# Performance work log

Hardware: AMD Instinct MI355X
Metric: run time of the kernel (lower is better)

The kernel has to match this reference:

```python
import jax, jax.numpy as jnp
import numpy as np

N_NODES = 100000
N_EDGES = 600000
IN_DIM, HID, OUT = 6, 128, 1
EPS = 1e-5


def _glorot(key, shape):
    fan_in, fan_out = shape[1], shape[0]
    lim = jnp.sqrt(6.0 / (fan_in + fan_out))
    return jax.random.uniform(key, shape, jnp.float32, -lim, lim)


def setup_inputs() -> dict:
    key = jax.random.key(0)
    ks = jax.random.split(key, 16)
    x = jax.random.normal(ks[0], (N_NODES, IN_DIM), jnp.float32)
    edge_index = jax.random.randint(ks[1], (2, N_EDGES), 0, N_NODES, jnp.int64)
    return {
        "x": x,
        "edge_index": edge_index,
        # SAGEConv layer 0: 6 -> 128 (lin_l acts on aggregated neighbors, lin_r on root)
        "w_l0": _glorot(ks[2], (HID, IN_DIM)), "b_l0": jnp.zeros((HID,), jnp.float32),
        "w_r0": _glorot(ks[3], (HID, IN_DIM)),
        "bn_g0": jnp.ones((HID,), jnp.float32), "bn_b0": jnp.zeros((HID,), jnp.float32),
        # SAGEConv layer 1: 128 -> 128
        "w_l1": _glorot(ks[4], (HID, HID)), "b_l1": jnp.zeros((HID,), jnp.float32),
        "w_r1": _glorot(ks[5], (HID, HID)),
        "bn_g1": jnp.ones((HID,), jnp.float32), "bn_b1": jnp.zeros((HID,), jnp.float32),
        # SAGEConv layer 2: 128 -> 1
        "w_l2": _glorot(ks[6], (OUT, HID)), "b_l2": jnp.zeros((OUT,), jnp.float32),
        "w_r2": _glorot(ks[7], (OUT, HID)),
    }


def _sage_conv(x, src, dst, inv_deg, w_l, b_l, w_r):
    # mean aggregation of source-node features into destination nodes
    agg = jax.ops.segment_sum(x[src], dst, num_segments=N_NODES)  # [N, d]
    mean_nb = agg * inv_deg[:, None]
    return mean_nb @ w_l.T + b_l + x @ w_r.T


def _batch_norm(x, gamma, beta):
    mu = jnp.mean(x, axis=0)
    var = jnp.mean(jnp.square(x - mu), axis=0)  # biased, as torch BN training
    return (x - mu) * jax.lax.rsqrt(var + EPS) * gamma + beta


def reference(x, edge_index, w_l0, b_l0, w_r0, bn_g0, bn_b0,
              w_l1, b_l1, w_r1, bn_g1, bn_b1, w_l2, b_l2, w_r2):
    src, dst = edge_index[0], edge_index[1]
    deg = jax.ops.segment_sum(jnp.ones_like(dst, dtype=x.dtype), dst,
                              num_segments=N_NODES)
    inv_deg = 1.0 / jnp.maximum(deg, 1.0)

    h = _sage_conv(x, src, dst, inv_deg, w_l0, b_l0, w_r0)
    h = jax.nn.relu(_batch_norm(h, bn_g0, bn_b0))  # dropout = identity (eval)

    h = _sage_conv(h, src, dst, inv_deg, w_l1, b_l1, w_r1)
    h = jax.nn.relu(_batch_norm(h, bn_g1, bn_b1))

    h = _sage_conv(h, src, dst, inv_deg, w_l2, b_l2, w_r2)
    return jax.nn.sigmoid(h).squeeze(-1)  # [N]
```

## Files before the change

### kernel.cpp

```cpp
#include <hip/hip_runtime.h>
#include <math.h>

#define HID 128
#define INDIM 6

typedef float4 f4;
typedef __attribute__((ext_vector_type(8))) short short8;
typedef __attribute__((ext_vector_type(4))) float f32x4;

static __device__ inline unsigned short f2bf(float f) {
    union { float f; unsigned int u; } v; v.f = f;
    unsigned int r = v.u + 0x7fffu + ((v.u >> 16) & 1u);
    return (unsigned short)(r >> 16);
}
static __device__ inline float bf2f_lo(unsigned int u) {
    union { unsigned int u; float f; } v; v.u = u << 16; return v.f;
}
static __device__ inline float bf2f_hi(unsigned int u) {
    union { unsigned int u; float f; } v; v.u = u & 0xffff0000u; return v.f;
}

__global__ void k_init(int* a, int na, int* b, int nb,
                       const float* __restrict__ wl, const float* __restrict__ wr,
                       unsigned short* __restrict__ wcat) {
    int i = blockIdx.x * blockDim.x + threadIdx.x;
    if (i < na) a[i] = 0;
    if (i < nb) b[i] = 0;
    if (i < 32768) {
        int o = i >> 8, k = i & 255;
        float v = (k < 128) ? wl[o * 128 + k] : wr[o * 128 + k - 128];
        wcat[i] = f2bf(v);
    }
}

__global__ void k_deg(const int* dst, int* deg, int* rank, int E) {
    int e = blockIdx.x * blockDim.x + threadIdx.x;
    if (e < E) rank[e] = atomicAdd(&deg[dst[e]], 1);
}

__global__ void k_scan_partial(const int* __restrict__ deg, int* __restrict__ partial, int N) {
    __shared__ int lds[256];
    int t = threadIdx.x;
    int base = blockIdx.x * 1024 + t * 4;
    int s = 0;
    if (base + 4 <= N) {
        int4 v = *(const int4*)&deg[base];
        s = v.x + v.y + v.z + v.w;
    } else {
        for (int i = 0; i < 4; i++) if (base + i < N) s += deg[base + i];
    }
    lds[t] = s;
    __syncthreads();
    for (int off = 128; off > 0; off >>= 1) {
        if (t < off) lds[t] += lds[t + off];
        __syncthreads();
    }
    if (t == 0) partial[blockIdx.x] = lds[0];
}

__global__ void k_scan_write(const int* __restrict__ deg, const int* __restrict__ partial,
                             int* __restrict__ rowptr, float* __restrict__ invd,
                             int N, int E, int nb) {
    __shared__ int lds[256];
    __shared__ int ptot[256];
    int t = threadIdx.x;
    ptot[t] = (t < nb) ? partial[t] : 0;
    __syncthreads();
    for (int off = 1; off < 256; off <<= 1) {
        int v = (t >= off) ? ptot[t - off] : 0;
        __syncthreads();
        ptot[t] += v;
        __syncthreads();
    }
    int blockbase = (blockIdx.x == 0) ? 0 : ptot[blockIdx.x - 1];

    int base = blockIdx.x * 1024 + t * 4;
    int v0 = 0, v1 = 0, v2 = 0, v3 = 0;
    if (base + 4 <= N) {
        int4 v = *(const int4*)&deg[base];
        v0 = v.x; v1 = v.y; v2 = v.z; v3 = v.w;
    } else {
        if (base + 0 < N) v0 = deg[base + 0];
        if (base + 1 < N) v1 = deg[base + 1];
        if (base + 2 < N) v2 = deg[base + 2];
        if (base + 3 < N) v3 = deg[base + 3];
    }
    lds[t] = v0 + v1 + v2 + v3;
    __syncthreads();
    for (int off = 1; off < 256; off <<= 1) {
        int v = (t >= off) ? lds[t - off] : 0;
        __syncthreads();
        lds[t] += v;
        __syncthreads();
    }
    int run = blockbase + ((t == 0) ? 0 : lds[t - 1]);
    if (base + 0 < N) { rowptr[base + 0] = run; invd[base + 0] = 1.0f / (float)max(v0, 1); } run += v0;
    if (base + 1 < N) { rowptr[base + 1] = run; invd[base + 1] = 1.0f / (float)max(v1, 1); } run += v1;
    if (base + 2 < N) { rowptr[base + 2] = run; invd[base + 2] = 1.0f / (float)max(v2, 1); } run += v2;
    if (base + 3 < N) { rowptr[base + 3] = run; invd[base + 3] = 1.0f / (float)max(v3, 1); } run += v3;
    if (blockIdx.x == 0 && t == 0) rowptr[N] = E;
}

__global__ void k_fill(const int* ei, const int* rank, const int* rowptr, int* csr, int E) {
    int e = blockIdx.x * blockDim.x + threadIdx.x;
    if (e < E) {
        int d = ei[E + e];
        csr[rowptr[d] + rank[e]] = ei[e];
    }
}

__global__ __launch_bounds__(256) void k_l0stats(
        const float* __restrict__ x, const int* __restrict__ rowptr,
        const int* __restrict__ csr, const float* __restrict__ invd,
        const float* __restrict__ wl, const float* __restrict__ bl,
        const float* __restrict__ wr, float* __restrict__ mean6,
        float* __restrict__ sum8, float* __restrict__ sq8, int N) {
    __shared__ float wlds[1600];
    __shared__ float blds[136];
    __shared__ float mx[32][8];
    __shared__ float xr[32][8];
    __shared__ float ps[4][128];
    __shared__ float pq[4][128];
    int t = threadIdx.x;
    for (int idx = t; idx < 1536; idx += 256) {
        int half = idx >= 768 ? 1 : 0;
        int lin = idx - half * 768;
        int o = lin / 6, i = lin - o * 6;
        float v = half ? wr[lin] : wl[lin];
        wlds[half * 800 + o * 6 + i + (o >> 4) * 2] = v;
    }
    if (t < 128) blds[t + (t >> 4)] = bl[t];
    int nl = t >> 3, f = t & 7;
    int n = blockIdx.x * 32 + nl;
    bool valid = n < N;
    if (f < 6) {
        float mean = 0.f, xv = 0.f;
        if (valid) {
            int s = rowptr[n], e = rowptr[n + 1];
            float acc = 0.f;
            int i = s;
            for (; i + 4 <= e; i += 4) {
                int i0 = csr[i], i1 = csr[i + 1], i2 = csr[i + 2], i3 = csr[i + 3];
                float a0 = x[i0 * 6 + f], a1 = x[i1 * 6 + f];
                float a2 = x[i2 * 6 + f], a3 = x[i3 * 6 + f];
                acc += (a0 + a1) + (a2 + a3);
            }
            int rem = e - i;
            if (rem > 0) {
                int eL = e - 1;
                int i0 = csr[i];
                int i1 = csr[min(i + 1, eL)];
                int i2 = csr[min(i + 2, eL)];
                float a0 = x[i0 * 6 + f];
                float a1 = x[i1 * 6 + f];
                float a2 = x[i2 * 6 + f];
                acc += a0;
                if (rem > 1) acc += a1;
                if (rem > 2) acc += a2;
            }
            mean = acc * invd[n];
            xv = x[n * 6 + f];
            mean6[n * 6 + f] = mean;
        }
        mx[nl][f] = mean;
        xr[nl][f] = xv;
    }
    __syncthreads();
    float m0 = mx[nl][0], m1 = mx[nl][1], m2 = mx[nl][2];
    float m3 = mx[nl][3], m4 = mx[nl][4], m5 = mx[nl][5];
    float r0 = xr[nl][0], r1 = xr[nl][1], r2 = xr[nl][2];
    float r3 = xr[nl][3], r4 = xr[nl][4], r5 = xr[nl][5];
    const float* wA = wlds;
    const float* wB = wlds + 800;
    int wv = t >> 6, lane = t & 63;
#pragma unroll
    for (int k = 0; k < 16; k++) {
        int o = f * 16 + k;
        int wb = 98 * f + 6 * k;
        float h = blds[o + f];
        h += m0 * wA[wb] + m1 * wA[wb + 1] + m2 * wA[wb + 2]
           + m3 * wA[wb + 3] + m4 * wA[wb + 4] + m5 * wA[wb + 5];
        h += r0 * wB[wb] + r1 * wB[wb + 1] + r2 * wB[wb + 2]
           + r3 * wB[wb + 3] + r4 * wB[wb + 4] + r5 * wB[wb + 5];
        float s = valid ? h : 0.f;
        float q = s * s;
        s += __shfl_xor(s, 8, 64);  q += __shfl_xor(q, 8, 64);
        s += __shfl_xor(s, 16, 64); q += __shfl_xor(q, 16, 64);
        s += __shfl_xor(s, 32, 64); q += __shfl_xor(q, 32, 64);
        if (lane < 8) { ps[wv][lane * 16 + k] = s; pq[wv][lane * 16 + k] = q; }
    }
    __syncthreads();
    if (t < 128) {
        float S = ps[0][t] + ps[1][t] + ps[2][t] + ps[3][t];
        float Q = pq[0][t] + pq[1][t] + pq[2][t] + pq[3][t];
        int slot = (blockIdx.x & 7) * 128 + t;
        atomicAdd(&sum8[slot], S);
        atomicAdd(&sq8[slot], Q);
    }
}

__global__ __launch_bounds__(256) void k_l0apply(
        const float* __restrict__ x, const float* __restrict__ mean6,
        const float* __restrict__ wl, const float* __restrict__ bl,
        const float* __restrict__ wr, const float* __restrict__ sum8,
        const float* __restrict__ sq8, const float* __restrict__ g,
        const float* __restrict__ be, float invN,
        unsigned short* __restrict__ out, int N) {
    __shared__ float wlds[1600];
    __shared__ float blds[136];
    __shared__ float sclds[136];
    __shared__ float shlds[136];
    __shared__ float mx[32][8];
    __shared__ float xr[32][8];
    int t = threadIdx.x;
    for (int idx = t; idx < 1536; idx += 256) {
        int half = idx >= 768 ? 1 : 0;
        int lin = idx - half * 768;
        int o = lin / 6, i = lin - o * 6;
        float v = half ? wr[lin] : wl[lin];
        wlds[half * 800 + o * 6 + i + (o >> 4) * 2] = v;
    }
    if (t < 128) {
        blds[t + (t >> 4)] = bl[t];
        float s = 0.f, q = 0.f;
        for (int c = 0; c < 8; c++) { s += sum8[c * 128 + t]; q += sq8[c * 128 + t]; }
        float mu  = s * invN;
        float var = q * invN - mu * mu;
        float sc  = g[t] * rsqrtf(var + 1e-5f);
        sclds[t + (t >> 4)] = sc;
        shlds[t + (t >> 4)] = be[t] - mu * sc;
    }
    int nl = t >> 3, f = t & 7;
    int n = blockIdx.x * 32 + nl;
    bool valid = n < N;
    if (f < 6) {
        mx[nl][f] = valid ? mean6[n * 6 + f] : 0.f;
        xr[nl][f] = valid ? x[n * 6 + f] : 0.f;
    }
    __syncthreads();
    if (!valid) return;
    float m0 = mx[nl][0], m1 = mx[nl][1], m2 = mx[nl][2];
    float m3 = mx[nl][3], m4 = mx[nl][4], m5 = mx[nl][5];
    float r0 = xr[nl][0], r1 = xr[nl][1], r2 = xr[nl][2];
    float r3 = xr[nl][3], r4 = xr[nl][4], r5 = xr[nl][5];
    const float* wA = wlds;
    const float* wB = wlds + 800;
    unsigned short pk[16];
#pragma unroll
    for (int k4 = 0; k4 < 4; k4++) {
#pragma unroll
        for (int j = 0; j < 4; j++) {
            int k = k4 * 4 + j;
            int o = f * 16 + k;
            int wb = 98 * f + 6 * k;
            float h = blds[o + f];
            h += m0 * wA[wb] + m1 * wA[wb + 1] + m2 * wA[wb + 2]
               + m3 * wA[wb + 3] + m4 * wA[wb + 4] + m5 * wA[wb + 5];
            h += r0 * wB[wb] + r1 * wB[wb + 1] + r2 * wB[wb + 2]
               + r3 * wB[wb + 3] + r4 * wB[wb + 4] + r5 * wB[wb + 5];
            pk[k] = f2bf(fmaxf(0.f, fmaf(h, sclds[o + f], shlds[o + f])));
        }
    }
    unsigned short* dst = out + (size_t)n * HID + f * 16;
    *(uint4*)(dst)     = *(const uint4*)&pk[0];
    *(uint4*)(dst + 8) = *(const uint4*)&pk[8];
}

__global__ void k_agg_bf(const unsigned short* __restrict__ hb, const int* __restrict__ rowptr,
                         const int* __restrict__ csr, const float* __restrict__ invd,
                         unsigned short* __restrict__ out, int N) {
    int t = threadIdx.x;
    int w = t >> 6, lid = t & 63;
    int q = lid >> 4, l16 = lid & 15;
    int n = blockIdx.x * 16 + w * 4 + q;
    if (n >= N) return;
    int s = rowptr[n], e = rowptr[n + 1];
    const uint4* hb128 = (const uint4*)hb;
    float ax0 = 0.f, ay0 = 0.f, ax1 = 0.f, ay1 = 0.f;
    float ax2 = 0.f, ay2 = 0.f, ax3 = 0.f, ay3 = 0.f;
    int i = s;
    for (; i + 4 <= e; i += 4) {
        int i0 = csr[i], i1 = csr[i + 1], i2 = csr[i + 2], i3 = csr[i + 3];
        uint4 u0 = hb128[(size_t)i0 * 16 + l16];
        uint4 u1 = hb128[(size_t)i1 * 16 + l16];
        uint4 u2 = hb128[(size_t)i2 * 16 + l16];
        uint4 u3 = hb128[(size_t)i3 * 16 + l16];
        ax0 += (bf2f_lo(u0.x) + bf2f_lo(u1.x)) + (bf2f_lo(u2.x) + bf2f_lo(u3.x));
        ay0 += (bf2f_hi(u0.x) + bf2f_hi(u1.x)) + (bf2f_hi(u2.x) + bf2f_hi(u3.x));
        ax1 += (bf2f_lo(u0.y) + bf2f_lo(u1.y)) + (bf2f_lo(u2.y) + bf2f_lo(u3.y));
        ay1 += (bf2f_hi(u0.y) + bf2f_hi(u1.y)) + (bf2f_hi(u2.y) + bf2f_hi(u3.y));
        ax2 += (bf2f_lo(u0.z) + bf2f_lo(u1.z)) + (bf2f_lo(u2.z) + bf2f_lo(u3.z));
        ay2 += (bf2f_hi(u0.z) + bf2f_hi(u1.z)) + (bf2f_hi(u2.z) + bf2f_hi(u3.z));
        ax3 += (bf2f_lo(u0.w) + bf2f_lo(u1.w)) + (bf2f_lo(u2.w) + bf2f_lo(u3.w));
        ay3 += (bf2f_hi(u0.w) + bf2f_hi(u1.w)) + (bf2f_hi(u2.w) + bf2f_hi(u3.w));
    }
    int rem = e - i;
    if (rem > 0) {
        int eL = e - 1;
        int i0 = csr[i];
        int i1 = csr[min(i + 1, eL)];
        int i2 = csr[min(i + 2, eL)];
        uint4 u0 = hb128[(size_t)i0 * 16 + l16];
        uint4 u1 = hb128[(size_t)i1 * 16 + l16];
        uint4 u2 = hb128[(size_t)i2 * 16 + l16];
        ax0 += bf2f_lo(u0.x); ay0 += bf2f_hi(u0.x);
        ax1 += bf2f_lo(u0.y); ay1 += bf2f_hi(u0.y);
        ax2 += bf2f_lo(u0.z); ay2 += bf2f_hi(u0.z);
        ax3 += bf2f_lo(u0.w); ay3 += bf2f_hi(u0.w);
        if (rem > 1) {
            ax0 += bf2f_lo(u1.x); ay0 += bf2f_hi(u1.x);
            ax1 += bf2f_lo(u1.y); ay1 += bf2f_hi(u1.y);
            ax2 += bf2f_lo(u1.z); ay2 += bf2f_hi(u1.z);
            ax3 += bf2f_lo(u1.w); ay3 += bf2f_hi(u1.w);
        }
        if (rem > 2) {
            ax0 += bf2f_lo(u2.x); ay0 += bf2f_hi(u2.x);
            ax1 += bf2f_lo(u2.y); ay1 += bf2f_hi(u2.y);
            ax2 += bf2f_lo(u2.z); ay2 += bf2f_hi(u2.z);
            ax3 += bf2f_lo(u2.w); ay3 += bf2f_hi(u2.w);
        }
    }
    float id = invd[n];
    uint4 r;
    r.x = (unsigned int)f2bf(ax0 * id) | ((unsigned int)f2bf(ay0 * id) << 16);
    r.y = (unsigned int)f2bf(ax1 * id) | ((unsigned int)f2bf(ay1 * id) << 16);
    r.z = (unsigned int)f2bf(ax2 * id) | ((unsigned int)f2bf(ay2 * id) << 16);
    r.w = (unsigned int)f2bf(ax3 * id) | ((unsigned int)f2bf(ay3 * id) << 16);
    ((uint4*)out)[(size_t)n * 16 + l16] = r;
}

__global__ __launch_bounds__(256) void k_gemm(
        const unsigned short* __restrict__ Bm, const unsigned short* __restrict__ Ar,
        const unsigned short* __restrict__ wcat, const float* __restrict__ bias,
        float* __restrict__ sum8, float* __restrict__ sq8,
        unsigned short* __restrict__ C, int N) {
    __shared__ __align__(16) unsigned short As[64][72];
    __shared__ __align__(16) unsigned short Ws[128][72];
    __shared__ float lds_s[128];
    __shared__ float lds_q[128];
    int t = threadIdx.x;
    int wave = t >> 6, lane = t & 63;
    int row0 = blockIdx.x * 64;
    int lrow = lane & 15, koff = (lane >> 4) * 8;

    f32x4 acc[4][2];
#pragma unroll
    for (int m = 0; m < 4; m++)
#pragma unroll
        for (int n = 0; n < 2; n++) acc[m][n] = (f32x4)(0.f);

    for (int chunk = 0; chunk < 4; chunk++) {
        int kb = chunk * 64;
        int rA = t >> 2, qA = t & 3;
        int srow = row0 + rA;
        int cA = (kb & 127) + qA * 16;
        const unsigned short* src = (kb < 128) ? Bm : Ar;
        uint4 a0, a1;
        if (srow < N) {
            const unsigned short* p = src + (size_t)srow * HID + cA;
            a0 = *(const uint4*)(p); a1 = *(const uint4*)(p + 8);
        } else {
            a0 = a1 = make_uint4(0, 0, 0, 0);
        }
        *(uint4*)&As[rA][qA * 16]     = a0;
        *(uint4*)&As[rA][qA * 16 + 8] = a1;
        int rW = t >> 1, hW = t & 1;
        const unsigned short* wp = wcat + rW * 256 + kb + hW * 32;
        *(uint4*)&Ws[rW][hW * 32]      = *(const uint4*)(wp);
        *(uint4*)&Ws[rW][hW * 32 + 8]  = *(const uint4*)(wp + 8);
        *(uint4*)&Ws[rW][hW * 32 + 16] = *(const uint4*)(wp + 16);
        *(uint4*)&Ws[rW][hW * 32 + 24] = *(const uint4*)(wp + 24);
        __syncthreads();

#pragma unroll
        for (int ks = 0; ks < 64; ks += 32) {
            short8 af[4], bfr[2];
#pragma unroll
            for (int m = 0; m < 4; m++)
                af[m] = *(const short8*)&As[m * 16 + lrow][ks + koff];
#pragma unroll
            for (int n = 0; n < 2; n++)
                bfr[n] = *(const short8*)&Ws[wave * 32 + n * 16 + lrow][ks + koff];
#pragma unroll
            for (int m = 0; m < 4; m++)
#pragma unroll
                for (int n = 0; n < 2; n++)
                    acc[m][n] = __builtin_amdgcn_mfma_f32_16x16x32_bf16(af[m], bfr[n], acc[m][n], 0, 0, 0);
        }
        __syncthreads();
    }

    unsigned short* Cst = &Ws[0][0];
    int cl = lane & 15, rq = (lane >> 4) * 4;
#pragma unroll
    for (int n = 0; n < 2; n++) {
        int col = wave * 32 + n * 16 + cl;
        float bn = bias[col];
        float s = 0.f, q = 0.f;
#pragma unroll
        for (int m = 0; m < 4; m++) {
#pragma unroll
            for (int reg = 0; reg < 4; reg++) {
                int rl = m * 16 + rq + reg;
                float v = acc[m][n][reg] + bn;
                Cst[rl * 136 + col] = f2bf(v);
                if (row0 + rl < N) { s += v; q += v * v; }
            }
        }
        s += __shfl_xor(s, 16, 64); q += __shfl_xor(q, 16, 64);
        s += __shfl_xor(s, 32, 64); q += __shfl_xor(q, 32, 64);
        if (lane < 16) { lds_s[col] = s; lds_q[col] = q; }
    }
    __syncthreads();
    if (t < 128) {
        int slot = (blockIdx.x & 7) * 128 + t;
        atomicAdd(&sum8[slot], lds_s[t]);
        atomicAdd(&sq8[slot], lds_q[t]);
    }
#pragma unroll
    for (int j = 0; j < 4; j++) {
        int idx = t + j * 256;
        int rl = idx >> 4, seg = idx & 15;
        int row = row0 + rl;
        if (row < N)
            *(uint4*)(C + (size_t)row * HID + seg * 8) = *(const uint4*)&Cst[rl * 136 + seg * 8];
    }
}

__global__ void k_dots(const unsigned short* __restrict__ h, const float* __restrict__ sum8,
                       const float* __restrict__ sq8, const float* __restrict__ g,
                       const float* __restrict__ be, float invN,
                       const float* __restrict__ wl2, const float* __restrict__ wr2,
                       float* __restrict__ s_arr, float* __restrict__ r_arr, int N) {
    __shared__ float scl[128];
    __shared__ float shl[128];
    int t = threadIdx.x;
    if (t < 128) {
        float s = 0.f, q = 0.f;
        for (int c = 0; c < 8; c++) { s += sum8[c * 128 + t]; q += sq8[c * 128 + t]; }
        float mu  = s * invN;
        float var = q * invN - mu * mu;
        float sc  = g[t] * rsqrtf(var + 1e-5f);
        scl[t] = sc;
        shl[t] = be[t] - mu * sc;
    }
    __syncthreads();
    int w = t >> 6, lid = t & 63;
    int n = blockIdx.x * 4 + w;
    if (n >= N) return;
    unsigned int u = ((const unsigned int*)h)[(size_t)n * 64 + lid];
    float hx = bf2f_lo(u), hy = bf2f_hi(u);
    float2 sc = *(const float2*)&scl[lid * 2];
    float2 sh = *(const float2*)&shl[lid * 2];
    float y0 = fmaxf(0.f, fmaf(hx, sc.x, sh.x));
    float y1 = fmaxf(0.f, fmaf(hy, sc.y, sh.y));
    float2 wl = *(const float2*)&wl2[lid * 2];
    float2 wrv = *(const float2*)&wr2[lid * 2];
    float ps = y0 * wl.x + y1 * wl.y;
    float pr = y0 * wrv.x + y1 * wrv.y;
#pragma unroll
    for (int off = 32; off > 0; off >>= 1) {
        ps += __shfl_down(ps, off, 64);
        pr += __shfl_down(pr, off, 64);
    }
    if (lid == 0) { s_arr[n] = ps; r_arr[n] = pr; }
}

__global__ void k_final2(const float* __restrict__ s_arr, const float* __restrict__ r_arr,
                         const int* __restrict__ rowptr, const int* __restrict__ csr,
                         const float* __restrict__ invd, const float* __restrict__ bl2,
                         float* __restrict__ out, int N) {
    int n = blockIdx.x * blockDim.x + threadIdx.x;
    if (n >= N) return;
    int s = rowptr[n], e = rowptr[n + 1];
    float a = 0.f;
    int i = s;
    for (; i + 4 <= e; i += 4) {
        float a0 = s_arr[csr[i]],     a1 = s_arr[csr[i + 1]];
        float a2 = s_arr[csr[i + 2]], a3 = s_arr[csr[i + 3]];
        a += (a0 + a1) + (a2 + a3);
    }
    int rem = e - i;
    if (rem > 0) {
        int eL = e - 1;
        float a0 = s_arr[csr[i]];
        float a1 = s_arr[csr[min(i + 1, eL)]];
        float a2 = s_arr[csr[min(i + 2, eL)]];
        a += a0;
        if (rem > 1) a += a1;
        if (rem > 2) a += a2;
    }
    float p = a * invd[n] + r_arr[n] + bl2[0];
    out[n] = 1.f / (1.f + expf(-p));
}

extern "C" void kernel_launch(void* const* d_in, const int* in_sizes, int n_in,
                              void* d_out, int out_size, void* d_ws, size_t ws_size,
                              hipStream_t stream) {
    const float* x   = (const float*)d_in[0];
    const int*   ei  = (const int*)d_in[1];
    const float* wl0 = (const float*)d_in[2];
    const float* bl0 = (const float*)d_in[3];
    const float* wr0 = (const float*)d_in[4];
    const float* g0  = (const float*)d_in[5];
    const float* be0 = (const float*)d_in[6];
    const float* wl1 = (const float*)d_in[7];
    const float* bl1 = (const float*)d_in[8];
    const float* wr1 = (const float*)d_in[9];
    const float* g1  = (const float*)d_in[10];
    const float* be1 = (const float*)d_in[11];
    const float* wl2 = (const float*)d_in[12];
    const float* bl2 = (const float*)d_in[13];
    const float* wr2 = (const float*)d_in[14];
    float* outp = (float*)d_out;

    int N = in_sizes[0] / INDIM;
    int E = in_sizes[1] / 2;

    char* ws = (char*)d_ws;
    size_t off = 0;
    auto alloc = [&](size_t bytes) { size_t o = off; off = (off + bytes + 255) & ~(size_t)255; return o; };
    int*   degi   = (int*)(ws + alloc((size_t)N * 4));
    int*   rank   = (int*)(ws + alloc((size_t)E * 4));
    int*   rowptr = (int*)(ws + alloc((size_t)(N + 1) * 4));
    int*   csr    = (int*)(ws + alloc((size_t)E * 4));
    float* invd   = (float*)(ws + alloc((size_t)N * 4));
    int*   partial= (int*)(ws + alloc(1024 * 4));
    float* bnbuf  = (float*)(ws + alloc(5120 * 4));
    unsigned short* wcat = (unsigned short*)(ws + alloc(128 * 256 * 2));
    float* sarr   = (float*)(ws + alloc((size_t)N * 4));
    float* rarr   = (float*)(ws + alloc((size_t)N * 4));
    float* mean6  = (float*)(ws + alloc((size_t)N * 6 * 4));
    float* sum0_8 = bnbuf;
    float* sq0_8  = bnbuf + 1024;
    float* sum1_8 = bnbuf + 2048;
    float* sq1_8  = bnbuf + 3072;
    unsigned short* bufB = (unsigned short*)(ws + alloc((size_t)N * HID * 2));
    unsigned short* bufC = (unsigned short*)(ws + alloc((size_t)N * HID * 2));
    unsigned short* bufD = (unsigned short*)(ws + alloc((size_t)N * HID * 2));

    float invN = 1.0f / (float)N;
    int gE = (E + 255) / 256;
    int gN = (N + 255) / 256;
    int gW = (N + 3) / 4;
    int gA = (N + 15) / 16;
    int gL = (N + 31) / 32;
    int gS = (N + 63) / 64;
    int nbScan = (N + 1023) / 1024;

    k_init<<<gN, 256, 0, stream>>>(degi, N, (int*)bnbuf, 4096, wl1, wr1, wcat);

    k_deg<<<gE, 256, 0, stream>>>(ei + E, degi, rank, E);
    k_scan_partial<<<nbScan, 256, 0, stream>>>(degi, partial, N);
    k_scan_write<<<nbScan, 256, 0, stream>>>(degi, partial, rowptr, invd, N, E, nbScan);
    k_fill<<<gE, 256, 0, stream>>>(ei, rank, rowptr, csr, E);

    k_l0stats<<<gL, 256, 0, stream>>>(x, rowptr, csr, invd, wl0, bl0, wr0, mean6,
                                      sum0_8, sq0_8, N);

    k_l0apply<<<gL, 256, 0, stream>>>(x, mean6, wl0, bl0, wr0,
                                      sum0_8, sq0_8, g0, be0, invN, bufC, N);

    k_agg_bf<<<gA, 256, 0, stream>>>(bufC, rowptr, csr, invd, bufD, N);
    k_gemm<<<gS, 256, 0, stream>>>(bufD, bufC, wcat, bl1, sum1_8, sq1_8, bufB, N);

    k_dots<<<gW, 256, 0, stream>>>(bufB, sum1_8, sq1_8, g1, be1, invN, wl2, wr2,
                                   sarr, rarr, N);
    k_final2<<<gN, 256, 0, stream>>>(sarr, rarr, rowptr, csr, invd, bl2, outp, N);
}
```

Before: 179.6 us.

## Fuse layer-1 neighbor aggregation into the GEMM kernel via shared memory

The layer-1 mean aggregation is now computed inside the GEMM kernel. Each block gathers the neighbor means for its 64 rows straight into a 64x136 LDS tile, which the MFMA loop then reads for the first half of K. This removes one kernel launch and the write and re-read of the N x 128 bf16 intermediate buffer. In exchange, the GEMM block now carries the irregular gather latency before its matrix work, with fewer rows per wave in flight and more LDS per block, which may lower occupancy.

```diff
diff --git a/kernel.cpp b/kernel.cpp
--- a/kernel.cpp
+++ b/kernel.cpp
@@ -266,75 +266,13 @@
     *(uint4*)(dst + 8) = *(const uint4*)&pk[8];
 }
 
-__global__ void k_agg_bf(const unsigned short* __restrict__ hb, const int* __restrict__ rowptr,
-                         const int* __restrict__ csr, const float* __restrict__ invd,
-                         unsigned short* __restrict__ out, int N) {
-    int t = threadIdx.x;
-    int w = t >> 6, lid = t & 63;
-    int q = lid >> 4, l16 = lid & 15;
-    int n = blockIdx.x * 16 + w * 4 + q;
-    if (n >= N) return;
-    int s = rowptr[n], e = rowptr[n + 1];
-    const uint4* hb128 = (const uint4*)hb;
-    float ax0 = 0.f, ay0 = 0.f, ax1 = 0.f, ay1 = 0.f;
-    float ax2 = 0.f, ay2 = 0.f, ax3 = 0.f, ay3 = 0.f;
-    int i = s;
-    for (; i + 4 <= e; i += 4) {
-        int i0 = csr[i], i1 = csr[i + 1], i2 = csr[i + 2], i3 = csr[i + 3];
-        uint4 u0 = hb128[(size_t)i0 * 16 + l16];
-        uint4 u1 = hb128[(size_t)i1 * 16 + l16];
-        uint4 u2 = hb128[(size_t)i2 * 16 + l16];
-        uint4 u3 = hb128[(size_t)i3 * 16 + l16];
-        ax0 += (bf2f_lo(u0.x) + bf2f_lo(u1.x)) + (bf2f_lo(u2.x) + bf2f_lo(u3.x));
-        ay0 += (bf2f_hi(u0.x) + bf2f_hi(u1.x)) + (bf2f_hi(u2.x) + bf2f_hi(u3.x));
-        ax1 += (bf2f_lo(u0.y) + bf2f_lo(u1.y)) + (bf2f_lo(u2.y) + bf2f_lo(u3.y));
-        ay1 += (bf2f_hi(u0.y) + bf2f_hi(u1.y)) + (bf2f_hi(u2.y) + bf2f_hi(u3.y));
-        ax2 += (bf2f_lo(u0.z) + bf2f_lo(u1.z)) + (bf2f_lo(u2.z) + bf2f_lo(u3.z));
-        ay2 += (bf2f_hi(u0.z) + bf2f_hi(u1.z)) + (bf2f_hi(u2.z) + bf2f_hi(u3.z));
-        ax3 += (bf2f_lo(u0.w) + bf2f_lo(u1.w)) + (bf2f_lo(u2.w) + bf2f_lo(u3.w));
-        ay3 += (bf2f_hi(u0.w) + bf2f_hi(u1.w)) + (bf2f_hi(u2.w) + bf2f_hi(u3.w));
-    }
-    int rem = e - i;
-    if (rem > 0) {
-        int eL = e - 1;
-        int i0 = csr[i];
-        int i1 = csr[min(i + 1, eL)];
-        int i2 = csr[min(i + 2, eL)];
-        uint4 u0 = hb128[(size_t)i0 * 16 + l16];
-        uint4 u1 = hb128[(size_t)i1 * 16 + l16];
-        uint4 u2 = hb128[(size_t)i2 * 16 + l16];
-        ax0 += bf2f_lo(u0.x); ay0 += bf2f_hi(u0.x);
-        ax1 += bf2f_lo(u0.y); ay1 += bf2f_hi(u0.y);
-        ax2 += bf2f_lo(u0.z); ay2 += bf2f_hi(u0.z);
-        ax3 += bf2f_lo(u0.w); ay3 += bf2f_hi(u0.w);
-        if (rem > 1) {
-            ax0 += bf2f_lo(u1.x); ay0 += bf2f_hi(u1.x);
-            ax1 += bf2f_lo(u1.y); ay1 += bf2f_hi(u1.y);
-            ax2 += bf2f_lo(u1.z); ay2 += bf2f_hi(u1.z);
-            ax3 += bf2f_lo(u1.w); ay3 += bf2f_hi(u1.w);
-        }
-        if (rem > 2) {
-            ax0 += bf2f_lo(u2.x); ay0 += bf2f_hi(u2.x);
-            ax1 += bf2f_lo(u2.y); ay1 += bf2f_hi(u2.y);
-            ax2 += bf2f_lo(u2.z); ay2 += bf2f_hi(u2.z);
-            ax3 += bf2f_lo(u2.w); ay3 += bf2f_hi(u2.w);
-        }
-    }
-    float id = invd[n];
-    uint4 r;
-    r.x = (unsigned int)f2bf(ax0 * id) | ((unsigned int)f2bf(ay0 * id) << 16);
-    r.y = (unsigned int)f2bf(ax1 * id) | ((unsigned int)f2bf(ay1 * id) << 16);
-    r.z = (unsigned int)f2bf(ax2 * id) | ((unsigned int)f2bf(ay2 * id) << 16);
-    r.w = (unsigned int)f2bf(ax3 * id) | ((unsigned int)f2bf(ay3 * id) << 16);
-    ((uint4*)out)[(size_t)n * 16 + l16] = r;
-}
-
-__global__ __launch_bounds__(256) void k_gemm(
-        const unsigned short* __restrict__ Bm, const unsigned short* __restrict__ Ar,
+__global__ __launch_bounds__(256) void k_agggemm(
+        const unsigned short* __restrict__ hb, const int* __restrict__ rowptr,
+        const int* __restrict__ csr, const float* __restrict__ invd,
         const unsigned short* __restrict__ wcat, const float* __restrict__ bias,
         float* __restrict__ sum8, float* __restrict__ sq8,
         unsigned short* __restrict__ C, int N) {
-    __shared__ __align__(16) unsigned short As[64][72];
+    __shared__ __align__(16) unsigned short Am[64][136];
     __shared__ __align__(16) unsigned short Ws[128][72];
     __shared__ float lds_s[128];
     __shared__ float lds_q[128];
@@ -342,6 +280,69 @@
     int wave = t >> 6, lane = t & 63;
     int row0 = blockIdx.x * 64;
     int lrow = lane & 15, koff = (lane >> 4) * 8;
+    int qtr = lane >> 4, l16 = lane & 15;
+
+    const uint4* hb128 = (const uint4*)hb;
+    for (int it = 0; it < 4; it++) {
+        int nl = wave * 16 + it * 4 + qtr;
+        int n = row0 + nl;
+        if (n < N) {
+            int s = rowptr[n], e = rowptr[n + 1];
+            float ax0 = 0.f, ay0 = 0.f, ax1 = 0.f, ay1 = 0.f;
+            float ax2 = 0.f, ay2 = 0.f, ax3 = 0.f, ay3 = 0.f;
+            int i = s;
+            for (; i + 4 <= e; i += 4) {
+                int i0 = csr[i], i1 = csr[i + 1], i2 = csr[i + 2], i3 = csr[i + 3];
+                uint4 u0 = hb128[(size_t)i0 * 16 + l16];
+                uint4 u1 = hb128[(size_t)i1 * 16 + l16];
+                uint4 u2 = hb128[(size_t)i2 * 16 + l16];
+                uint4 u3 = hb128[(size_t)i3 * 16 + l16];
+                ax0 += (bf2f_lo(u0.x) + bf2f_lo(u1.x)) + (bf2f_lo(u2.x) + bf2f_lo(u3.x));
+                ay0 += (bf2f_hi(u0.x) + bf2f_hi(u1.x)) + (bf2f_hi(u2.x) + bf2f_hi(u3.x));
+                ax1 += (bf2f_lo(u0.y) + bf2f_lo(u1.y)) + (bf2f_lo(u2.y) + bf2f_lo(u3.y));
+                ay1 += (bf2f_hi(u0.y) + bf2f_hi(u1.y)) + (bf2f_hi(u2.y) + bf2f_hi(u3.y));
+                ax2 += (bf2f_lo(u0.z) + bf2f_lo(u1.z)) + (bf2f_lo(u2.z) + bf2f_lo(u3.z));
+                ay2 += (bf2f_hi(u0.z) + bf2f_hi(u1.z)) + (bf2f_hi(u2.z) + bf2f_hi(u3.z));
+                ax3 += (bf2f_lo(u0.w) + bf2f_lo(u1.w)) + (bf2f_lo(u2.w) + bf2f_lo(u3.w));
+                ay3 += (bf2f_hi(u0.w) + bf2f_hi(u1.w)) + (bf2f_hi(u2.w) + bf2f_hi(u3.w));
+            }
+            int rem = e - i;
+            if (rem > 0) {
+                int eL = e - 1;
+                int i0 = csr[i];
+                int i1 = csr[min(i + 1, eL)];
+                int i2 = csr[min(i + 2, eL)];
+                uint4 u0 = hb128[(size_t)i0 * 16 + l16];
+                uint4 u1 = hb128[(size_t)i1 * 16 + l16];
+                uint4 u2 = hb128[(size_t)i2 * 16 + l16];
+                ax0 += bf2f_lo(u0.x); ay0 += bf2f_hi(u0.x);
+                ax1 += bf2f_lo(u0.y); ay1 += bf2f_hi(u0.y);
+                ax2 += bf2f_lo(u0.z); ay2 += bf2f_hi(u0.z);
+                ax3 += bf2f_lo(u0.w); ay3 += bf2f_hi(u0.w);
+                if (rem > 1) {
+                    ax0 += bf2f_lo(u1.x); ay0 += bf2f_hi(u1.x);
+                    ax1 += bf2f_lo(u1.y); ay1 += bf2f_hi(u1.y);
+                    ax2 += bf2f_lo(u1.z); ay2 += bf2f_hi(u1.z);
+                    ax3 += bf2f_lo(u1.w); ay3 += bf2f_hi(u1.w);
+                }
+                if (rem > 2) {
+                    ax0 += bf2f_lo(u2.x); ay0 += bf2f_hi(u2.x);
+                    ax1 += bf2f_lo(u2.y); ay1 += bf2f_hi(u2.y);
+                    ax2 += bf2f_lo(u2.z); ay2 += bf2f_hi(u2.z);
+                    ax3 += bf2f_lo(u2.w); ay3 += bf2f_hi(u2.w);
+                }
+            }
+            float id = invd[n];
+            uint4 r;
+            r.x = (unsigned int)f2bf(ax0 * id) | ((unsigned int)f2bf(ay0 * id) << 16);
+            r.y = (unsigned int)f2bf(ax1 * id) | ((unsigned int)f2bf(ay1 * id) << 16);
+            r.z = (unsigned int)f2bf(ax2 * id) | ((unsigned int)f2bf(ay2 * id) << 16);
+            r.w = (unsigned int)f2bf(ax3 * id) | ((unsigned int)f2bf(ay3 * id) << 16);
+            *(uint4*)&Am[nl][l16 * 8] = r;
+        } else {
+            *(uint4*)&Am[nl][l16 * 8] = make_uint4(0, 0, 0, 0);
+        }
+    }
 
     f32x4 acc[4][2];
 #pragma unroll
@@ -351,19 +352,20 @@
 
     for (int chunk = 0; chunk < 4; chunk++) {
         int kb = chunk * 64;
-        int rA = t >> 2, qA = t & 3;
-        int srow = row0 + rA;
-        int cA = (kb & 127) + qA * 16;
-        const unsigned short* src = (kb < 128) ? Bm : Ar;
-        uint4 a0, a1;
-        if (srow < N) {
-            const unsigned short* p = src + (size_t)srow * HID + cA;
-            a0 = *(const uint4*)(p); a1 = *(const uint4*)(p + 8);
-        } else {
-            a0 = a1 = make_uint4(0, 0, 0, 0);
+        if (chunk >= 2) {
+            int rA = t >> 2, qA = t & 3;
+            int srow = row0 + rA;
+            int cA = (kb & 127) + qA * 16;
+            uint4 a0, a1;
+            if (srow < N) {
+                const unsigned short* p = hb + (size_t)srow * HID + cA;
+                a0 = *(const uint4*)(p); a1 = *(const uint4*)(p + 8);
+            } else {
+                a0 = a1 = make_uint4(0, 0, 0, 0);
+            }
+            *(uint4*)&Am[rA][qA * 16]     = a0;
+            *(uint4*)&Am[rA][qA * 16 + 8] = a1;
         }
-        *(uint4*)&As[rA][qA * 16]     = a0;
-        *(uint4*)&As[rA][qA * 16 + 8] = a1;
         int rW = t >> 1, hW = t & 1;
         const unsigned short* wp = wcat + rW * 256 + kb + hW * 32;
         *(uint4*)&Ws[rW][hW * 32]      = *(const uint4*)(wp);
@@ -372,12 +374,13 @@
         *(uint4*)&Ws[rW][hW * 32 + 24] = *(const uint4*)(wp + 24);
         __syncthreads();
 
+        int acol = (chunk < 2) ? kb : 0;
 #pragma unroll
         for (int ks = 0; ks < 64; ks += 32) {
             short8 af[4], bfr[2];
 #pragma unroll
             for (int m = 0; m < 4; m++)
-                af[m] = *(const short8*)&As[m * 16 + lrow][ks + koff];
+                af[m] = *(const short8*)&Am[m * 16 + lrow][acol + ks + koff];
 #pragma unroll
             for (int n = 0; n < 2; n++)
                 bfr[n] = *(const short8*)&Ws[wave * 32 + n * 16 + lrow][ks + koff];
@@ -390,7 +393,7 @@
         __syncthreads();
     }
 
-    unsigned short* Cst = &Ws[0][0];
+    unsigned short* Cst = &Am[0][0];
     int cl = lane & 15, rq = (lane >> 4) * 4;
 #pragma unroll
     for (int n = 0; n < 2; n++) {
@@ -537,13 +540,11 @@
     float* sq1_8  = bnbuf + 3072;
     unsigned short* bufB = (unsigned short*)(ws + alloc((size_t)N * HID * 2));
     unsigned short* bufC = (unsigned short*)(ws + alloc((size_t)N * HID * 2));
-    unsigned short* bufD = (unsigned short*)(ws + alloc((size_t)N * HID * 2));
 
     float invN = 1.0f / (float)N;
     int gE = (E + 255) / 256;
     int gN = (N + 255) / 256;
     int gW = (N + 3) / 4;
-    int gA = (N + 15) / 16;
     int gL = (N + 31) / 32;
     int gS = (N + 63) / 64;
     int nbScan = (N + 1023) / 1024;
@@ -561,8 +562,8 @@
     k_l0apply<<<gL, 256, 0, stream>>>(x, mean6, wl0, bl0, wr0,
                                       sum0_8, sq0_8, g0, be0, invN, bufC, N);
 
-    k_agg_bf<<<gA, 256, 0, stream>>>(bufC, rowptr, csr, invd, bufD, N);
-    k_gemm<<<gS, 256, 0, stream>>>(bufD, bufC, wcat, bl1, sum1_8, sq1_8, bufB, N);
+    k_agggemm<<<gS, 256, 0, stream>>>(bufC, rowptr, csr, invd, wcat, bl1,
+                                      sum1_8, sq1_8, bufB, N);
 
     k_dots<<<gW, 256, 0, stream>>>(bufB, sum1_8, sq1_8, g1, be1, invN, wl2, wr2,
                                    sarr, rarr, N);
```

After: 178.6 us. About the same (-0.6%).
